# Kernel optimization log

Measured on AMD Instinct MI355X. Metric: run time of the kernel, lower is better.

## Reference

```python
import jax, jax.numpy as jnp
import numpy as np

D_MODEL = 1024
N_HEADS = 16
D_HEAD = D_MODEL // N_HEADS


def setup_inputs() -> dict:
    key = jax.random.key(0)
    k_x, k_q, k_k, k_v, k_o = jax.random.split(key, 5)
    scale = 1.0 / np.sqrt(D_MODEL)
    return {
        "x": jax.random.normal(k_x, (4, 2048, D_MODEL), dtype=jnp.float32),
        "W_Q": jax.random.normal(k_q, (D_MODEL, D_MODEL), dtype=jnp.float32) * scale,
        "W_K": jax.random.normal(k_k, (D_MODEL, D_MODEL), dtype=jnp.float32) * scale,
        "W_V": jax.random.normal(k_v, (D_MODEL, D_MODEL), dtype=jnp.float32) * scale,
        "W_O": jax.random.normal(k_o, (D_MODEL, D_MODEL), dtype=jnp.float32) * scale,
    }


def _split_heads(t):
    B, T, D = t.shape
    return t.reshape(B, T, N_HEADS, D_HEAD).transpose(0, 2, 1, 3)  # [B,H,T,Dh]


def reference(x, W_Q, W_K, W_V, W_O):
    B, T, D = x.shape
    # nn.Linear(d,d,bias=False): y = x @ W.T
    q = _split_heads(x @ W_Q.T)
    k = _split_heads(x @ W_K.T)
    v = _split_heads(x @ W_V.T)
    scores = jnp.einsum("bhqd,bhkd->bhqk", q, k) / np.sqrt(D_HEAD).astype(np.float32)
    causal = jnp.tril(jnp.ones((T, T), dtype=bool))
    scores = jnp.where(causal[None, None], scores, jnp.finfo(scores.dtype).min)
    attn = jax.nn.softmax(scores, axis=-1)  # dropout p=0.0 -> identity
    head_out = jnp.einsum("bhqk,bhkd->bhqd", attn, v)
    merged = head_out.transpose(0, 2, 1, 3).reshape(B, T, D)
    out = merged @ W_O.T
    return out
```

## Files before the change

### kernel.cpp

```cpp
#include <hip/hip_runtime.h>
#include <hip/hip_bf16.h>
#include <cstdint>
#include <cstddef>

typedef __bf16 bf16;
typedef __bf16 bf16x8 __attribute__((ext_vector_type(8)));
typedef __bf16 bf16x4 __attribute__((ext_vector_type(4)));
typedef __bf16 bf16x2 __attribute__((ext_vector_type(2)));
typedef float  f32x4  __attribute__((ext_vector_type(4)));
typedef float  f32x16 __attribute__((ext_vector_type(16)));
typedef unsigned int u32x2 __attribute__((ext_vector_type(2)));
typedef unsigned int u32x4 __attribute__((ext_vector_type(4)));

constexpr int D_MODEL = 1024;
constexpr int TT      = 2048;
constexpr int NBATCH  = 4;
constexpr int NH      = 16;
constexpr float C2   = 0.125f * 1.44269504088896340736f;
constexpr float M0C2 = 16.0f * C2;

typedef const __attribute__((address_space(1))) unsigned int* gas_ptr;
typedef       __attribute__((address_space(3))) unsigned int* las_ptr;

__device__ __forceinline__ void gload_lds16(const void* g, void* l) {
  __builtin_amdgcn_global_load_lds((gas_ptr)g, (las_ptr)l, 16, 0, 0);
}

__device__ __forceinline__ void permswap(unsigned int& a, unsigned int& b) {
  u32x2 r = __builtin_amdgcn_permlane32_swap(a, b, false, false);
  a = r[0]; b = r[1];
}

__device__ __forceinline__ unsigned int pk2(float a, float b) {
  bf16x2 t; t[0] = (bf16)a; t[1] = (bf16)b;
  return __builtin_bit_cast(unsigned int, t);
}

__global__ void cvt_kernel(const float* __restrict__ src, bf16* __restrict__ dst, int n4) {
  int i = blockIdx.x * blockDim.x + threadIdx.x;
  if (i < n4) {
    f32x4 v = reinterpret_cast<const f32x4*>(src)[i];
    bf16x4 o;
    o[0] = (bf16)v[0]; o[1] = (bf16)v[1]; o[2] = (bf16)v[2]; o[3] = (bf16)v[3];
    reinterpret_cast<bf16x4*>(dst)[i] = o;
  }
}

__global__ void cvt4_kernel(const float* __restrict__ a, const float* __restrict__ b,
                            const float* __restrict__ c, const float* __restrict__ d,
                            bf16* __restrict__ oa, bf16* __restrict__ ob,
                            bf16* __restrict__ oc, bf16* __restrict__ od) {
  const int i = blockIdx.x * 256 + threadIdx.x;
  const int g = i >> 18;
  const int k = i & ((1 << 18) - 1);
  const float* s = (g == 0) ? a : (g == 1) ? b : (g == 2) ? c : d;
  bf16*       o = (g == 0) ? oa : (g == 1) ? ob : (g == 2) ? oc : od;
  f32x4 v = reinterpret_cast<const f32x4*>(s)[k];
  bf16x4 t;
  t[0] = (bf16)v[0]; t[1] = (bf16)v[1]; t[2] = (bf16)v[2]; t[3] = (bf16)v[3];
  reinterpret_cast<bf16x4*>(o)[k] = t;
}

template<int OM>
__global__ void gemm_nt(const bf16* __restrict__ A, const bf16* __restrict__ B,
                        void* __restrict__ C, int N) {
  constexpr int KD = 1024;
  __shared__ __align__(16) bf16 At[128 * 32];
  __shared__ __align__(16) bf16 Bt[128 * 32];

  const int tid = threadIdx.x;
  const int w  = tid >> 6, l = tid & 63;
  const int lr = l & 15,  lh = l >> 4;
  const int wr = w >> 1,  wc = w & 1;
  const long brow = (long)blockIdx.x * 128;
  const long bcol = (long)blockIdx.y * 128;

  const int seg_r = l >> 2;
  const int seg_c = (l & 3) * 8;

  f32x4 acc[4][4] = {};

  for (int kk = 0; kk < KD; kk += 32) {
    __syncthreads();
    #pragma unroll
    for (int i = 0; i < 2; ++i) {
      const int seg = w * 2 + i;
      const int row = seg * 16 + seg_r;
      gload_lds16(A + (brow + row) * KD + kk + seg_c, At + seg * 512);
      gload_lds16(B + (bcol + row) * KD + kk + seg_c, Bt + seg * 512);
    }
    __syncthreads();

    bf16x8 af[4], bfr[4];
    #pragma unroll
    for (int m = 0; m < 4; ++m)
      af[m] = *reinterpret_cast<const bf16x8*>(At + (wr * 64 + m * 16 + lr) * 32 + lh * 8);
    #pragma unroll
    for (int n = 0; n < 4; ++n)
      bfr[n] = *reinterpret_cast<const bf16x8*>(Bt + (wc * 64 + n * 16 + lr) * 32 + lh * 8);
    #pragma unroll
    for (int m = 0; m < 4; ++m)
      #pragma unroll
      for (int n = 0; n < 4; ++n)
        acc[m][n] = __builtin_amdgcn_mfma_f32_16x16x32_bf16(af[m], bfr[n], acc[m][n], 0, 0, 0);
  }

  #pragma unroll
  for (int m = 0; m < 4; ++m) {
    #pragma unroll
    for (int n = 0; n < 4; ++n) {
      #pragma unroll
      for (int j = 0; j < 4; ++j) {
        const long gr = brow + wr * 64 + m * 16 + lh * 4 + j;
        const long gc = bcol + wc * 64 + n * 16 + lr;
        const float v = acc[m][n][j];
        if constexpr (OM == 1) ((float*)C)[gr * (long)N + gc] = v;
        else                   ((bf16*)C)[gr * (long)N + gc] = (bf16)v;
      }
    }
  }
}

__global__ __launch_bounds__(256, 2)
void flash_kernel(const bf16* __restrict__ Q, const bf16* __restrict__ K,
                  const bf16* __restrict__ Vt, bf16* __restrict__ Om) {
  const int bh  = blockIdx.x;
  const int qtA = 8 + blockIdx.y;
  const int qtB = 15 - qtA;
  const int b   = bh >> 4, h = bh & 15;
  const int tid = threadIdx.x;
  const int w   = tid >> 6, l = tid & 63;
  const int l31 = l & 31;
  const int h5  = l >> 5;

  __shared__ __align__(16) bf16 Kl[2][64 * 64];
  __shared__ __align__(16) bf16 Vl[2][64 * 64];

  const int qt_[2] = {qtA, qtB};

  bf16x8 qf[2][4];
  #pragma unroll
  for (int t = 0; t < 2; ++t) {
    const bf16* qp = Q + ((long)(b * TT + qt_[t] * 128 + w * 32 + l31)) * D_MODEL + h * 64 + h5 * 8;
    #pragma unroll
    for (int k16 = 0; k16 < 4; ++k16)
      qf[t][k16] = *reinterpret_cast<const bf16x8*>(qp + k16 * 16);
  }

  f32x16 acc[2][2] = {};
  float  lp[2] = {};

  auto stage = [&](int kt, int p) {
    #pragma unroll
    for (int i = 0; i < 2; ++i) {
      const int ch = i * 256 + w * 64 + l;
      const int r  = ch >> 3;
      const int c  = (ch & 7) ^ (r & 7);
      gload_lds16(K  + ((long)(b * TT + kt * 64 + r)) * D_MODEL + h * 64 + c * 8,
                  (bf16*)Kl[p] + (i * 4 + w) * 512);
      gload_lds16(Vt + ((long)(h * 64 + r)) * (NBATCH * TT) + b * TT + kt * 64 + c * 8,
                  (bf16*)Vl[p] + (i * 4 + w) * 512);
    }
  };

  const int NTA = 2 * qtA + 2, NTB = 2 * qtB + 2;
  stage(0, 0);
  __syncthreads();
  int cur = 0;

  for (int kt = 0; kt < NTA; ++kt) {
    if (kt + 1 < NTA) stage(kt + 1, cur ^ 1);

    bf16x8 kf[2][4];
    #pragma unroll
    for (int kb = 0; kb < 2; ++kb) {
      const int row = kb * 32 + l31;
      #pragma unroll
      for (int k16 = 0; k16 < 4; ++k16)
        kf[kb][k16] = *reinterpret_cast<const bf16x8*>(
            (char*)Kl[cur] + row * 128 + ((k16 * 32 + h5 * 16) ^ ((row & 7) << 4)));
    }
    bf16x8 vf[4][2];
    #pragma unroll
    for (int db = 0; db < 2; ++db) {
      const int row = db * 32 + l31;
      #pragma unroll
      for (int k4 = 0; k4 < 4; ++k4)
        vf[k4][db] = *reinterpret_cast<const bf16x8*>(
            (char*)Vl[cur] + row * 128 + ((k4 * 32 + h5 * 16) ^ ((row & 7) << 4)));
    }

    #pragma unroll
    for (int t = 0; t < 2; ++t) {
      if (t == 1 && kt >= NTB) continue;
      const bool diag = (kt >= 2 * qt_[t]);

      f32x16 s[2] = {};
      #pragma unroll
      for (int kb = 0; kb < 2; ++kb)
        #pragma unroll
        for (int k16 = 0; k16 < 4; ++k16)
          s[kb] = __builtin_amdgcn_mfma_f32_32x32x16_bf16(kf[kb][k16], qf[t][k16], s[kb], 0, 0, 0);

      const int qrow = qt_[t] * 128 + w * 32 + l31;
      float lsum = 0.f;
      unsigned int W[2][8];
      #pragma unroll
      for (int kb = 0; kb < 2; ++kb) {
        #pragma unroll
        for (int pr = 0; pr < 8; ++pr) {
          const int r0 = 2 * pr;
          float p0 = __builtin_exp2f(C2 * s[kb][r0]     - M0C2);
          float p1 = __builtin_exp2f(C2 * s[kb][r0 + 1] - M0C2);
          if (diag) {
            const int kv0 = kt * 64 + kb * 32 + (r0 & 3) + 8 * (r0 >> 2) + 4 * h5;
            if (kv0     > qrow) p0 = 0.f;
            if (kv0 + 1 > qrow) p1 = 0.f;
          }
          lsum += p0 + p1;
          W[kb][pr] = pk2(p0, p1);
        }
      }
      lp[t] += lsum;

      #pragma unroll
      for (int k4 = 0; k4 < 4; ++k4) {
        const int kb = k4 >> 1, u = (k4 & 1) * 4;
        unsigned int a0 = W[kb][u + 0], b0 = W[kb][u + 2];
        unsigned int a1 = W[kb][u + 1], b1 = W[kb][u + 3];
        permswap(a0, b0);
        permswap(a1, b1);
        u32x4 paw; paw[0] = a0; paw[1] = a1; paw[2] = b0; paw[3] = b1;
        const bf16x8 pa = __builtin_bit_cast(bf16x8, paw);
        #pragma unroll
        for (int db = 0; db < 2; ++db)
          acc[t][db] = __builtin_amdgcn_mfma_f32_32x32x16_bf16(pa, vf[k4][db], acc[t][db], 0, 0, 0);
      }
    }

    __syncthreads();
    cur ^= 1;
  }

  #pragma unroll
  for (int t = 0; t < 2; ++t) {
    float v = lp[t];
    v += __shfl_xor(v, 32, 64);
    const float li = 1.0f / v;
    #pragma unroll
    for (int r = 0; r < 16; ++r) {
      const int qloc = (r & 3) + 8 * (r >> 2) + 4 * h5;
      const float liw = __shfl(li, qloc, 64);
      const long row = (long)(b * TT + qt_[t] * 128 + w * 32 + qloc);
      #pragma unroll
      for (int db = 0; db < 2; ++db)
        Om[row * D_MODEL + h * 64 + db * 32 + l31] = (bf16)(acc[t][db][r] * liw);
    }
  }
}

extern "C" void kernel_launch(void* const* d_in, const int* in_sizes, int n_in,
                              void* d_out, int out_size, void* d_ws, size_t ws_size,
                              hipStream_t stream) {
  (void)in_sizes; (void)n_in; (void)out_size; (void)ws_size;
  const float* x  = (const float*)d_in[0];
  const float* Wq = (const float*)d_in[1];
  const float* Wk = (const float*)d_in[2];
  const float* Wv = (const float*)d_in[3];
  const float* Wo = (const float*)d_in[4];

  char* ws = (char*)d_ws;
  bf16* xb  = (bf16*)(ws);
  bf16* Wqb = (bf16*)(ws + (16u << 20));
  bf16* Wkb = (bf16*)(ws + (18u << 20));
  bf16* Wvb = (bf16*)(ws + (20u << 20));
  bf16* Wob = (bf16*)(ws + (22u << 20));
  bf16* Vt  = (bf16*)(ws + (24u << 20));
  bf16* Mrg = (bf16*)(ws + (40u << 20));
  bf16* Qb = (bf16*)d_out;
  bf16* Kb = Qb + (size_t)8192 * 1024;

  const int NX = NBATCH * TT * D_MODEL;
  cvt_kernel<<<(NX / 4 + 255) / 256, 256, 0, stream>>>(x, xb, NX / 4);
  cvt4_kernel<<<4096, 256, 0, stream>>>(Wq, Wk, Wv, Wo, Wqb, Wkb, Wvb, Wob);

  gemm_nt<0><<<dim3(64, 8), 256, 0, stream>>>(xb, Wqb, Qb, 1024);
  gemm_nt<0><<<dim3(64, 8), 256, 0, stream>>>(xb, Wkb, Kb, 1024);
  gemm_nt<0><<<dim3(8, 64), 256, 0, stream>>>(Wvb, xb, Vt, 8192);

  flash_kernel<<<dim3(NBATCH * NH, 8), 256, 0, stream>>>(Qb, Kb, Vt, Mrg);

  gemm_nt<1><<<dim3(64, 8), 256, 0, stream>>>(Mrg, Wob, d_out, 1024);
}
```

Before: 191.6 us.

## Fuse conversions and QK projections, compute softmax row sums via MFMA

Merges the x and weight fp32-to-bf16 conversions into one launch. Concatenates W_Q and W_K so one GEMM writes an interleaved QK buffer with row stride 2048. In the flash kernel it skips per-wave KV tiles that are fully masked for that wave's 32 query rows. It replaces the scalar row-sum accumulation with an extra MFMA against a ones vector, and it hoists the LDS swizzle offsets out of the loop. The ones-MFMA adds matrix-core work per tile, and the per-wave skip may cause divergence between waves at the barrier.

```diff
diff --git a/kernel.cpp b/kernel.cpp
--- a/kernel.cpp
+++ b/kernel.cpp
@@ -16,6 +16,7 @@
 constexpr int TT      = 2048;
 constexpr int NBATCH  = 4;
 constexpr int NH      = 16;
+constexpr int QKS     = 2048;
 constexpr float C2   = 0.125f * 1.44269504088896340736f;
 constexpr float M0C2 = 16.0f * C2;
 
@@ -36,25 +37,22 @@
   return __builtin_bit_cast(unsigned int, t);
 }
 
-__global__ void cvt_kernel(const float* __restrict__ src, bf16* __restrict__ dst, int n4) {
-  int i = blockIdx.x * blockDim.x + threadIdx.x;
-  if (i < n4) {
-    f32x4 v = reinterpret_cast<const f32x4*>(src)[i];
-    bf16x4 o;
-    o[0] = (bf16)v[0]; o[1] = (bf16)v[1]; o[2] = (bf16)v[2]; o[3] = (bf16)v[3];
-    reinterpret_cast<bf16x4*>(dst)[i] = o;
-  }
-}
-
-__global__ void cvt4_kernel(const float* __restrict__ a, const float* __restrict__ b,
-                            const float* __restrict__ c, const float* __restrict__ d,
-                            bf16* __restrict__ oa, bf16* __restrict__ ob,
-                            bf16* __restrict__ oc, bf16* __restrict__ od) {
+__global__ void cvtall_kernel(const float* __restrict__ x,  const float* __restrict__ wq,
+                              const float* __restrict__ wk, const float* __restrict__ wv,
+                              const float* __restrict__ wo,
+                              bf16* __restrict__ xb,  bf16* __restrict__ wqk,
+                              bf16* __restrict__ wvb, bf16* __restrict__ wob) {
   const int i = blockIdx.x * 256 + threadIdx.x;
-  const int g = i >> 18;
-  const int k = i & ((1 << 18) - 1);
-  const float* s = (g == 0) ? a : (g == 1) ? b : (g == 2) ? c : d;
-  bf16*       o = (g == 0) ? oa : (g == 1) ? ob : (g == 2) ? oc : od;
+  const float* s; bf16* o; int k;
+  if (i < (1 << 21)) {
+    s = x; o = xb; k = i;
+  } else {
+    const int j = i - (1 << 21);
+    const int g = j >> 18;
+    k = j & ((1 << 18) - 1);
+    s = (g == 0) ? wq : (g == 1) ? wk : (g == 2) ? wv : wo;
+    o = (g == 0) ? wqk : (g == 1) ? (wqk + (1u << 20)) : (g == 2) ? wvb : wob;
+  }
   f32x4 v = reinterpret_cast<const f32x4*>(s)[k];
   bf16x4 t;
   t[0] = (bf16)v[0]; t[1] = (bf16)v[1]; t[2] = (bf16)v[2]; t[3] = (bf16)v[3];
@@ -122,8 +120,8 @@
 }
 
 __global__ __launch_bounds__(256, 2)
-void flash_kernel(const bf16* __restrict__ Q, const bf16* __restrict__ K,
-                  const bf16* __restrict__ Vt, bf16* __restrict__ Om) {
+void flash_kernel(const bf16* __restrict__ QK, const bf16* __restrict__ Vt,
+                  bf16* __restrict__ Om) {
   const int bh  = blockIdx.x;
   const int qtA = 8 + blockIdx.y;
   const int qtB = 15 - qtA;
@@ -141,14 +139,34 @@
   bf16x8 qf[2][4];
   #pragma unroll
   for (int t = 0; t < 2; ++t) {
-    const bf16* qp = Q + ((long)(b * TT + qt_[t] * 128 + w * 32 + l31)) * D_MODEL + h * 64 + h5 * 8;
+    const bf16* qp = QK + ((long)(b * TT + qt_[t] * 128 + w * 32 + l31)) * QKS + h * 64 + h5 * 8;
     #pragma unroll
     for (int k16 = 0; k16 < 4; ++k16)
       qf[t][k16] = *reinterpret_cast<const bf16x8*>(qp + k16 * 16);
   }
 
+  bf16x8 onesf;
+  #pragma unroll
+  for (int e = 0; e < 8; ++e) onesf[e] = (bf16)1.0f;
+
   f32x16 acc[2][2] = {};
-  float  lp[2] = {};
+  f32x16 accl[2]  = {};
+
+  int koff[2][4], voff[4][2];
+  #pragma unroll
+  for (int kb = 0; kb < 2; ++kb) {
+    const int row = kb * 32 + l31;
+    #pragma unroll
+    for (int k16 = 0; k16 < 4; ++k16)
+      koff[kb][k16] = row * 128 + ((k16 * 32 + h5 * 16) ^ ((row & 7) << 4));
+  }
+  #pragma unroll
+  for (int db = 0; db < 2; ++db) {
+    const int row = db * 32 + l31;
+    #pragma unroll
+    for (int k4 = 0; k4 < 4; ++k4)
+      voff[k4][db] = row * 128 + ((k4 * 32 + h5 * 16) ^ ((row & 7) << 4));
+  }
 
   auto stage = [&](int kt, int p) {
     #pragma unroll
@@ -156,7 +174,7 @@
       const int ch = i * 256 + w * 64 + l;
       const int r  = ch >> 3;
       const int c  = (ch & 7) ^ (r & 7);
-      gload_lds16(K  + ((long)(b * TT + kt * 64 + r)) * D_MODEL + h * 64 + c * 8,
+      gload_lds16(QK + ((long)(b * TT + kt * 64 + r)) * QKS + 1024 + h * 64 + c * 8,
                   (bf16*)Kl[p] + (i * 4 + w) * 512);
       gload_lds16(Vt + ((long)(h * 64 + r)) * (NBATCH * TT) + b * TT + kt * 64 + c * 8,
                   (bf16*)Vl[p] + (i * 4 + w) * 512);
@@ -171,29 +189,27 @@
   for (int kt = 0; kt < NTA; ++kt) {
     if (kt + 1 < NTA) stage(kt + 1, cur ^ 1);
 
+    const char* kbase = (const char*)Kl[cur];
+    const char* vbase = (const char*)Vl[cur];
     bf16x8 kf[2][4];
     #pragma unroll
-    for (int kb = 0; kb < 2; ++kb) {
-      const int row = kb * 32 + l31;
+    for (int kb = 0; kb < 2; ++kb)
       #pragma unroll
       for (int k16 = 0; k16 < 4; ++k16)
-        kf[kb][k16] = *reinterpret_cast<const bf16x8*>(
-            (char*)Kl[cur] + row * 128 + ((k16 * 32 + h5 * 16) ^ ((row & 7) << 4)));
-    }
+        kf[kb][k16] = *reinterpret_cast<const bf16x8*>(kbase + koff[kb][k16]);
     bf16x8 vf[4][2];
     #pragma unroll
-    for (int db = 0; db < 2; ++db) {
-      const int row = db * 32 + l31;
-      #pragma unroll
-      for (int k4 = 0; k4 < 4; ++k4)
-        vf[k4][db] = *reinterpret_cast<const bf16x8*>(
-            (char*)Vl[cur] + row * 128 + ((k4 * 32 + h5 * 16) ^ ((row & 7) << 4)));
-    }
+    for (int k4 = 0; k4 < 4; ++k4)
+      #pragma unroll
+      for (int db = 0; db < 2; ++db)
+        vf[k4][db] = *reinterpret_cast<const bf16x8*>(vbase + voff[k4][db]);
 
     #pragma unroll
     for (int t = 0; t < 2; ++t) {
       if (t == 1 && kt >= NTB) continue;
-      const bool diag = (kt >= 2 * qt_[t]);
+      const int wq0 = qt_[t] * 128 + w * 32;
+      if (kt * 64 > wq0 + 31) continue;
+      const bool diag = (kt * 64 + 63 > wq0);
 
       f32x16 s[2] = {};
       #pragma unroll
@@ -202,8 +218,7 @@
         for (int k16 = 0; k16 < 4; ++k16)
           s[kb] = __builtin_amdgcn_mfma_f32_32x32x16_bf16(kf[kb][k16], qf[t][k16], s[kb], 0, 0, 0);
 
-      const int qrow = qt_[t] * 128 + w * 32 + l31;
-      float lsum = 0.f;
+      const int qrow = wq0 + l31;
       unsigned int W[2][8];
       #pragma unroll
       for (int kb = 0; kb < 2; ++kb) {
@@ -217,11 +232,9 @@
             if (kv0     > qrow) p0 = 0.f;
             if (kv0 + 1 > qrow) p1 = 0.f;
           }
-          lsum += p0 + p1;
           W[kb][pr] = pk2(p0, p1);
         }
       }
-      lp[t] += lsum;
 
       #pragma unroll
       for (int k4 = 0; k4 < 4; ++k4) {
@@ -232,6 +245,7 @@
         permswap(a1, b1);
         u32x4 paw; paw[0] = a0; paw[1] = a1; paw[2] = b0; paw[3] = b1;
         const bf16x8 pa = __builtin_bit_cast(bf16x8, paw);
+        accl[t] = __builtin_amdgcn_mfma_f32_32x32x16_bf16(pa, onesf, accl[t], 0, 0, 0);
         #pragma unroll
         for (int db = 0; db < 2; ++db)
           acc[t][db] = __builtin_amdgcn_mfma_f32_32x32x16_bf16(pa, vf[k4][db], acc[t][db], 0, 0, 0);
@@ -244,13 +258,10 @@
 
   #pragma unroll
   for (int t = 0; t < 2; ++t) {
-    float v = lp[t];
-    v += __shfl_xor(v, 32, 64);
-    const float li = 1.0f / v;
     #pragma unroll
     for (int r = 0; r < 16; ++r) {
       const int qloc = (r & 3) + 8 * (r >> 2) + 4 * h5;
-      const float liw = __shfl(li, qloc, 64);
+      const float liw = 1.0f / accl[t][r];
       const long row = (long)(b * TT + qt_[t] * 128 + w * 32 + qloc);
       #pragma unroll
       for (int db = 0; db < 2; ++db)
@@ -271,24 +282,20 @@
 
   char* ws = (char*)d_ws;
   bf16* xb  = (bf16*)(ws);
-  bf16* Wqb = (bf16*)(ws + (16u << 20));
-  bf16* Wkb = (bf16*)(ws + (18u << 20));
+  bf16* Wqk = (bf16*)(ws + (16u << 20));
   bf16* Wvb = (bf16*)(ws + (20u << 20));
   bf16* Wob = (bf16*)(ws + (22u << 20));
   bf16* Vt  = (bf16*)(ws + (24u << 20));
   bf16* Mrg = (bf16*)(ws + (40u << 20));
-  bf16* Qb = (bf16*)d_out;
-  bf16* Kb = Qb + (size_t)8192 * 1024;
-
-  const int NX = NBATCH * TT * D_MODEL;
-  cvt_kernel<<<(NX / 4 + 255) / 256, 256, 0, stream>>>(x, xb, NX / 4);
-  cvt4_kernel<<<4096, 256, 0, stream>>>(Wq, Wk, Wv, Wo, Wqb, Wkb, Wvb, Wob);
-
-  gemm_nt<0><<<dim3(64, 8), 256, 0, stream>>>(xb, Wqb, Qb, 1024);
-  gemm_nt<0><<<dim3(64, 8), 256, 0, stream>>>(xb, Wkb, Kb, 1024);
+  bf16* QKb = (bf16*)d_out;
+
+  cvtall_kernel<<<(3u << 20) / 256 * 1, 256, 0, stream>>>(x, Wq, Wk, Wv, Wo,
+                                                          xb, Wqk, Wvb, Wob);
+
+  gemm_nt<0><<<dim3(64, 16), 256, 0, stream>>>(xb, Wqk, QKb, 2048);
   gemm_nt<0><<<dim3(8, 64), 256, 0, stream>>>(Wvb, xb, Vt, 8192);
 
-  flash_kernel<<<dim3(NBATCH * NH, 8), 256, 0, stream>>>(Qb, Kb, Vt, Mrg);
+  flash_kernel<<<dim3(NBATCH * NH, 8), 256, 0, stream>>>(QKb, Vt, Mrg);
 
   gemm_nt<1><<<dim3(64, 8), 256, 0, stream>>>(Mrg, Wob, d_out, 1024);
 }
```

Result: no change. 189.4 us (-1.1%).
